# Kernel optimization log

Measured on AMD Instinct MI355X. Metric: run time of the kernel, lower is better.

The kernel has to match this reference:

```python
import jax, jax.numpy as jnp
import numpy as np

B, S, E, H, D = 2, 2048, 1024, 16, 64

def setup_inputs() -> dict:
    key = jax.random.key(0)
    ks = jax.random.split(key, 6)
    scale = 0.02
    x  = jax.random.normal(ks[0], (B, S, E), dtype=jnp.float32)
    Wq = jax.random.normal(ks[1], (E, E), dtype=jnp.float32) * scale
    Wk = jax.random.normal(ks[2], (E, E), dtype=jnp.float32) * scale
    Wv = jax.random.normal(ks[3], (E, E), dtype=jnp.float32) * scale
    Wo = jax.random.normal(ks[4], (E, E), dtype=jnp.float32) * scale
    bo = jax.random.normal(ks[5], (E,), dtype=jnp.float32) * scale
    return {"x": x, "Wq": Wq, "Wk": Wk, "Wv": Wv, "Wo": Wo, "bo": bo}

def reference(x, Wq, Wk, Wv, Wo, bo):
    # Per-head Q/K/V projections: equivalent to concatenating H heads of size D.
    q = jnp.einsum('bse,ehd->bhsd', x, Wq.reshape(E, H, D))
    k = jnp.einsum('bse,ehd->bhsd', x, Wk.reshape(E, H, D))
    v = jnp.einsum('bse,ehd->bhsd', x, Wv.reshape(E, H, D))
    # Scaled dot-product attention with causal mask (tril), per head.
    scores = jnp.einsum('bhqd,bhkd->bhqk', q, k) * (D ** -0.5)  # [B,H,S,S]
    causal = jnp.tril(jnp.ones((S, S), dtype=bool))
    scores = jnp.where(causal, scores, jnp.float32(-jnp.inf))
    attn = jax.nn.softmax(scores, axis=-1)
    out = jnp.einsum('bhqk,bhkd->bhqd', attn, v)            # [B,H,S,D]
    out = out.transpose(0, 2, 1, 3).reshape(B, S, E)        # concat heads
    # Output projection (dropout prob = 0.0 -> identity).
    return out @ Wo + bo
```

## Files before the change

kernel.cpp:

```cpp
#include <hip/hip_runtime.h>
#include <hip/hip_bf16.h>
#include <cstdint>
#include <cstddef>

typedef unsigned short u16;
typedef unsigned int u32;
typedef __bf16 bf16x8 __attribute__((ext_vector_type(8)));
typedef float f32x4 __attribute__((ext_vector_type(4)));
typedef u32 u32x4 __attribute__((ext_vector_type(4)));
typedef u32 u32x2 __attribute__((ext_vector_type(2)));

constexpr int Bb = 2, Ss = 2048, Ee = 1024, Hh = 16, Dd = 64;
constexpr int Mm = Bb * Ss;
constexpr int NT = Ss / 64;

__device__ __forceinline__ u16 f2bf(float f) {
    union { float f; u32 u; } x; x.f = f;
    u32 r = x.u + 0x7fffu + ((x.u >> 16) & 1u);
    return (u16)(r >> 16);
}

__global__ __launch_bounds__(256) void k_f2b(
    const float* __restrict__ src, u16* __restrict__ dst)
{
    const int i = blockIdx.x * 256 + threadIdx.x;
    float4 v = reinterpret_cast<const float4*>(src)[i];
    ushort4 o;
    o.x = f2bf(v.x); o.y = f2bf(v.y); o.z = f2bf(v.z); o.w = f2bf(v.w);
    reinterpret_cast<ushort4*>(dst)[i] = o;
}

__global__ __launch_bounds__(256) void k_transpose(
    const float* __restrict__ Wq, const float* __restrict__ Wk,
    const float* __restrict__ Wv, const float* __restrict__ Wo,
    u16* __restrict__ WqkvT, u16* __restrict__ WoT)
{
    __shared__ float sm[32][33];
    const int z = blockIdx.z;
    const float* src = (z == 0) ? Wq : (z == 1) ? Wk : (z == 2) ? Wv : Wo;
    u16* dst = (z < 3) ? (WqkvT + (size_t)z * Ee * Ee) : WoT;
    const int kt = blockIdx.x * 32, nt = blockIdx.y * 32;
    const int tx = threadIdx.x, ty = threadIdx.y;
#pragma unroll
    for (int i = 0; i < 4; ++i)
        sm[ty + 8 * i][tx] = src[(size_t)(kt + ty + 8 * i) * Ee + nt + tx];
    __syncthreads();
#pragma unroll
    for (int i = 0; i < 4; ++i)
        dst[(size_t)(nt + ty + 8 * i) * Ee + kt + tx] = f2bf(sm[tx][ty + 8 * i]);
}

template <int MODE>
__global__ __launch_bounds__(256) void k_gemm(
    const u16* __restrict__ A, const u16* __restrict__ Bt,
    void* __restrict__ Cout, u16* __restrict__ vT,
    int K, const float* __restrict__ bias)
{
    __shared__ u16 As[128][40];
    __shared__ u16 Bs[128][40];
    const int bm = blockIdx.x * 128, bn = blockIdx.y * 128;
    const int tid = threadIdx.x;
    const int wave = tid >> 6, lane = tid & 63, quad = lane >> 4, l16 = lane & 15;
    const int wr = wave >> 1, wc = wave & 1;

    f32x4 acc[4][4] = {};

    for (int k0 = 0; k0 < K; k0 += 32) {
#pragma unroll
        for (int it = 0; it < 2; ++it) {
            int v = tid + it * 256;
            int r = v >> 2, g = v & 3;
            *reinterpret_cast<int4*>(&As[r][g * 8]) =
                *reinterpret_cast<const int4*>(A + (size_t)(bm + r) * K + k0 + g * 8);
            *reinterpret_cast<int4*>(&Bs[r][g * 8]) =
                *reinterpret_cast<const int4*>(Bt + (size_t)(bn + r) * K + k0 + g * 8);
        }
        __syncthreads();

        bf16x8 af[4], bfr[4];
#pragma unroll
        for (int mt = 0; mt < 4; ++mt)
            af[mt] = *reinterpret_cast<bf16x8*>(&As[wr * 64 + mt * 16 + l16][quad * 8]);
#pragma unroll
        for (int nt = 0; nt < 4; ++nt)
            bfr[nt] = *reinterpret_cast<bf16x8*>(&Bs[wc * 64 + nt * 16 + l16][quad * 8]);
#pragma unroll
        for (int mt = 0; mt < 4; ++mt)
#pragma unroll
            for (int nt = 0; nt < 4; ++nt)
                acc[mt][nt] = __builtin_amdgcn_mfma_f32_16x16x32_bf16(
                    af[mt], bfr[nt], acc[mt][nt], 0, 0, 0);
        __syncthreads();
    }

    if constexpr (MODE == 1) {
        float* C = (float*)Cout;
#pragma unroll
        for (int mt = 0; mt < 4; ++mt)
#pragma unroll
            for (int nt = 0; nt < 4; ++nt) {
                const int col = bn + wc * 64 + nt * 16 + l16;
                const float bv = bias[col];
#pragma unroll
                for (int r = 0; r < 4; ++r) {
                    const int row = bm + wr * 64 + mt * 16 + quad * 4 + r;
                    C[(size_t)row * Ee + col] = acc[mt][nt][r] + bv;
                }
            }
    } else {
        if (bn < 2 * Ee) {
            u16* C = (u16*)Cout;
#pragma unroll
            for (int mt = 0; mt < 4; ++mt)
#pragma unroll
                for (int nt = 0; nt < 4; ++nt) {
                    const int col = bn + wc * 64 + nt * 16 + l16;
#pragma unroll
                    for (int r = 0; r < 4; ++r) {
                        const int row = bm + wr * 64 + mt * 16 + quad * 4 + r;
                        C[(size_t)row * (2 * Ee) + col] = f2bf(acc[mt][nt][r]);
                    }
                }
        } else {
#pragma unroll
            for (int mt = 0; mt < 4; ++mt)
#pragma unroll
                for (int nt = 0; nt < 4; ++nt) {
                    const int vd = bn - 2 * Ee + wc * 64 + nt * 16 + l16;
                    const int h = vd >> 6, d = vd & 63;
#pragma unroll
                    for (int r = 0; r < 4; ++r) {
                        const int row = bm + wr * 64 + mt * 16 + quad * 4 + r;
                        const int b = row >> 11, s = row & 2047;
                        vT[(((size_t)b * Hh + h) * Dd + d) * Ss + s] = f2bf(acc[mt][nt][r]);
                    }
                }
        }
    }
}

__global__ __launch_bounds__(256) void k_attn(
    const u16* __restrict__ qk, const u16* __restrict__ vT,
    u16* __restrict__ attn_out)
{
    __shared__ u16 Qs[64][72];
    __shared__ u16 Ks[2][64][72];
    __shared__ u16 Vs[2][64][72];

    const int pair = blockIdx.x;
    const int bh = blockIdx.y;
    const int b = bh >> 4, h = bh & 15;
    const int tid = threadIdx.x;
    const int wave = tid >> 6, lane = tid & 63, quad = lane >> 4, l16 = lane & 15;
    const int r8 = tid >> 3, g8 = tid & 7;
    const size_t qkbase = (size_t)b * Ss * (2 * Ee);
    const size_t vbase  = ((size_t)(b * Hh + h) * Dd) * Ss;

    const int tiles[2] = { pair, NT - 1 - pair };
    constexpr float LOG2E = 1.4426950408889634f;
    constexpr float C1 = 0.125f * LOG2E;
    constexpr float C2 = 4.0f * LOG2E;

    for (int ph = 0; ph < 2; ++ph) {
        const int qt = tiles[ph];

#pragma unroll
        for (int hf = 0; hf < 2; ++hf) {
            const int rr = r8 + hf * 32;
            *reinterpret_cast<int4*>(&Qs[rr][g8 * 8]) = *reinterpret_cast<const int4*>(
                qk + qkbase + (size_t)(qt * 64 + rr) * (2 * Ee) + h * 64 + g8 * 8);
            *reinterpret_cast<int4*>(&Ks[0][rr][g8 * 8]) = *reinterpret_cast<const int4*>(
                qk + qkbase + (size_t)rr * (2 * Ee) + Ee + h * 64 + g8 * 8);
            *reinterpret_cast<int4*>(&Vs[0][rr][g8 * 8]) = *reinterpret_cast<const int4*>(
                vT + vbase + (size_t)rr * Ss + g8 * 8);
        }
        __syncthreads();

        const bf16x8 aq0 = *reinterpret_cast<bf16x8*>(&Qs[wave * 16 + l16][quad * 8]);
        const bf16x8 aq1 = *reinterpret_cast<bf16x8*>(&Qs[wave * 16 + l16][32 + quad * 8]);

        float l_lane = 0.f;
        f32x4 acc[4];
#pragma unroll
        for (int dt = 0; dt < 4; ++dt) acc[dt] = (f32x4){0.f, 0.f, 0.f, 0.f};

        for (int kt = 0; kt <= qt; ++kt) {
            const int cur = kt & 1, nxt = cur ^ 1;
            int4 kreg0, kreg1, vreg0, vreg1;
            if (kt < qt) {
                kreg0 = *reinterpret_cast<const int4*>(
                    qk + qkbase + (size_t)((kt + 1) * 64 + r8) * (2 * Ee) + Ee + h * 64 + g8 * 8);
                kreg1 = *reinterpret_cast<const int4*>(
                    qk + qkbase + (size_t)((kt + 1) * 64 + r8 + 32) * (2 * Ee) + Ee + h * 64 + g8 * 8);
                vreg0 = *reinterpret_cast<const int4*>(
                    vT + vbase + (size_t)r8 * Ss + (kt + 1) * 64 + g8 * 8);
                vreg1 = *reinterpret_cast<const int4*>(
                    vT + vbase + (size_t)(r8 + 32) * Ss + (kt + 1) * 64 + g8 * 8);
            }

            f32x4 sc[4];
#pragma unroll
            for (int ct = 0; ct < 4; ++ct) {
                bf16x8 bk0 = *reinterpret_cast<bf16x8*>(&Ks[cur][ct * 16 + l16][quad * 8]);
                bf16x8 bk1 = *reinterpret_cast<bf16x8*>(&Ks[cur][ct * 16 + l16][32 + quad * 8]);
                f32x4 z = {0.f, 0.f, 0.f, 0.f};
                z = __builtin_amdgcn_mfma_f32_16x16x32_bf16(bk0, aq0, z, 0, 0, 0);
                z = __builtin_amdgcn_mfma_f32_16x16x32_bf16(bk1, aq1, z, 0, 0, 0);
                sc[ct] = z;
            }

            u32 pb[4][4];
            if (kt == qt) {
#pragma unroll
                for (int ct = 0; ct < 4; ++ct)
#pragma unroll
                    for (int r = 0; r < 4; ++r) {
                        float t = sc[ct][r] * C1 - C2;
                        if (ct * 16 + quad * 4 + r > wave * 16 + l16) t = -INFINITY;
                        union { float f; u32 u; } p; p.f = exp2f(t);
                        pb[ct][r] = p.u & 0xffff0000u;
                        p.u = pb[ct][r];
                        l_lane += p.f;
                    }
            } else {
#pragma unroll
                for (int ct = 0; ct < 4; ++ct)
#pragma unroll
                    for (int r = 0; r < 4; ++r) {
                        union { float f; u32 u; } p; p.f = exp2f(sc[ct][r] * C1 - C2);
                        pb[ct][r] = p.u & 0xffff0000u;
                        p.u = pb[ct][r];
                        l_lane += p.f;
                    }
            }

#pragma unroll
            for (int p2 = 0; p2 < 2; ++p2) {
                u32x4 bw;
                bw[0] = (pb[2 * p2][0] >> 16) | pb[2 * p2][1];
                bw[1] = (pb[2 * p2][2] >> 16) | pb[2 * p2][3];
                bw[2] = (pb[2 * p2 + 1][0] >> 16) | pb[2 * p2 + 1][1];
                bw[3] = (pb[2 * p2 + 1][2] >> 16) | pb[2 * p2 + 1][3];
                const bf16x8 pf = __builtin_bit_cast(bf16x8, bw);
#pragma unroll
                for (int dt = 0; dt < 4; ++dt) {
                    u32x2 lo = *reinterpret_cast<u32x2*>(&Vs[cur][dt * 16 + l16][p2 * 32 + quad * 4]);
                    u32x2 hi = *reinterpret_cast<u32x2*>(&Vs[cur][dt * 16 + l16][p2 * 32 + 16 + quad * 4]);
                    u32x4 aw = {lo[0], lo[1], hi[0], hi[1]};
                    const bf16x8 vf = __builtin_bit_cast(bf16x8, aw);
                    acc[dt] = __builtin_amdgcn_mfma_f32_16x16x32_bf16(vf, pf, acc[dt], 0, 0, 0);
                }
            }

            if (kt < qt) {
                *reinterpret_cast<int4*>(&Ks[nxt][r8][g8 * 8]) = kreg0;
                *reinterpret_cast<int4*>(&Ks[nxt][r8 + 32][g8 * 8]) = kreg1;
                *reinterpret_cast<int4*>(&Vs[nxt][r8][g8 * 8]) = vreg0;
                *reinterpret_cast<int4*>(&Vs[nxt][r8 + 32][g8 * 8]) = vreg1;
            }
            __syncthreads();
        }

        l_lane += __shfl_xor(l_lane, 16);
        l_lane += __shfl_xor(l_lane, 32);
        const float inv = 1.0f / l_lane;
        const int row = qt * 64 + wave * 16 + l16;
#pragma unroll
        for (int dt = 0; dt < 4; ++dt) {
            ushort4 o;
            o.x = f2bf(acc[dt][0] * inv);
            o.y = f2bf(acc[dt][1] * inv);
            o.z = f2bf(acc[dt][2] * inv);
            o.w = f2bf(acc[dt][3] * inv);
            *reinterpret_cast<ushort4*>(
                &attn_out[((size_t)b * Ss + row) * Ee + h * 64 + dt * 16 + quad * 4]) = o;
        }
    }
}

extern "C" void kernel_launch(void* const* d_in, const int* in_sizes, int n_in,
                              void* d_out, int out_size, void* d_ws, size_t ws_size,
                              hipStream_t stream)
{
    const float* x  = (const float*)d_in[0];
    const float* Wq = (const float*)d_in[1];
    const float* Wk = (const float*)d_in[2];
    const float* Wv = (const float*)d_in[3];
    const float* Wo = (const float*)d_in[4];
    const float* bo = (const float*)d_in[5];
    float* out = (float*)d_out;

    u16* xb    = (u16*)d_ws;
    u16* WqkvT = xb + (size_t)Mm * Ee;
    u16* WoT   = WqkvT + (size_t)3 * Ee * Ee;
    u16* qk    = WoT + (size_t)Ee * Ee;
    u16* vT    = qk + (size_t)Mm * 2 * Ee;
    u16* attn  = vT + (size_t)Bb * Hh * Dd * Ss;
    const size_t need = ((size_t)Mm * Ee + (size_t)3 * Ee * Ee + (size_t)Ee * Ee +
                         (size_t)Mm * 2 * Ee + (size_t)Bb * Hh * Dd * Ss +
                         (size_t)Mm * Ee) * sizeof(u16);
    if (ws_size < need) return;

    k_f2b<<<dim3(Mm * Ee / 4 / 256), 256, 0, stream>>>(x, xb);
    k_transpose<<<dim3(32, 32, 4), dim3(32, 8), 0, stream>>>(Wq, Wk, Wv, Wo, WqkvT, WoT);
    k_gemm<2><<<dim3(Mm / 128, 3 * Ee / 128), 256, 0, stream>>>(xb, WqkvT, qk, vT, Ee, nullptr);
    k_attn<<<dim3(NT / 2, Bb * Hh), 256, 0, stream>>>(qk, vT, attn);
    k_gemm<1><<<dim3(Mm / 128, Ee / 128), 256, 0, stream>>>(attn, WoT, out, nullptr, Ee, bo);
}
```

Measured before the change: 194.8 us.

## Fuse preprocessing kernels, use direct global-to-LDS loads, and coalesce V-transpose stores

Merges the x bf16 conversion and the weight transposes into one launch, with an extra z-slice handling the conversion. The GEMM tile loads now use global_load_lds to write straight into unpadded LDS tiles instead of passing through registers. The V-transposed epilogue goes through a per-wave LDS buffer so stores become 16-byte coalesced rows rather than scattered 2-byte writes. Side effects: the GEMM LDS tiles lose their padding, which may cause bank conflicts on fragment reads, and the loop still uses single buffering with barriers.

New measurement: 190.0 us. 2.5% less time.

```diff
diff --git a/kernel.cpp b/kernel.cpp
--- a/kernel.cpp
+++ b/kernel.cpp
@@ -20,27 +20,37 @@
     return (u16)(r >> 16);
 }
 
-__global__ __launch_bounds__(256) void k_f2b(
-    const float* __restrict__ src, u16* __restrict__ dst)
-{
-    const int i = blockIdx.x * 256 + threadIdx.x;
-    float4 v = reinterpret_cast<const float4*>(src)[i];
-    ushort4 o;
-    o.x = f2bf(v.x); o.y = f2bf(v.y); o.z = f2bf(v.z); o.w = f2bf(v.w);
-    reinterpret_cast<ushort4*>(dst)[i] = o;
-}
-
-__global__ __launch_bounds__(256) void k_transpose(
+typedef __attribute__((address_space(3))) void lds_void_t;
+typedef const __attribute__((address_space(1))) void gbl_void_t;
+__device__ __forceinline__ void gload_lds16(const u16* g, u16* l) {
+    __builtin_amdgcn_global_load_lds((gbl_void_t*)g, (lds_void_t*)l, 16, 0, 0);
+}
+
+__global__ __launch_bounds__(256) void k_pre(
+    const float* __restrict__ x,
     const float* __restrict__ Wq, const float* __restrict__ Wk,
     const float* __restrict__ Wv, const float* __restrict__ Wo,
-    u16* __restrict__ WqkvT, u16* __restrict__ WoT)
+    u16* __restrict__ xb, u16* __restrict__ WqkvT, u16* __restrict__ WoT)
 {
+    const int z = blockIdx.z;
+    const int tx = threadIdx.x, ty = threadIdx.y;
+    if (z == 4) {
+        const int tid = ty * 32 + tx;
+        const size_t base = ((size_t)blockIdx.y * 32 + blockIdx.x) * 4096;
+#pragma unroll
+        for (int it = 0; it < 4; ++it) {
+            const size_t i = base / 4 + it * 256 + tid;
+            float4 v = reinterpret_cast<const float4*>(x)[i];
+            ushort4 o;
+            o.x = f2bf(v.x); o.y = f2bf(v.y); o.z = f2bf(v.z); o.w = f2bf(v.w);
+            reinterpret_cast<ushort4*>(xb)[i] = o;
+        }
+        return;
+    }
     __shared__ float sm[32][33];
-    const int z = blockIdx.z;
     const float* src = (z == 0) ? Wq : (z == 1) ? Wk : (z == 2) ? Wv : Wo;
     u16* dst = (z < 3) ? (WqkvT + (size_t)z * Ee * Ee) : WoT;
     const int kt = blockIdx.x * 32, nt = blockIdx.y * 32;
-    const int tx = threadIdx.x, ty = threadIdx.y;
 #pragma unroll
     for (int i = 0; i < 4; ++i)
         sm[ty + 8 * i][tx] = src[(size_t)(kt + ty + 8 * i) * Ee + nt + tx];
@@ -56,25 +66,27 @@
     void* __restrict__ Cout, u16* __restrict__ vT,
     int K, const float* __restrict__ bias)
 {
-    __shared__ u16 As[128][40];
-    __shared__ u16 Bs[128][40];
+    __shared__ u16 As[128][32];
+    __shared__ u16 Bs[128][32];
+    __shared__ u16 Tw[4][16][68];
     const int bm = blockIdx.x * 128, bn = blockIdx.y * 128;
     const int tid = threadIdx.x;
     const int wave = tid >> 6, lane = tid & 63, quad = lane >> 4, l16 = lane & 15;
     const int wr = wave >> 1, wc = wave & 1;
 
+    const int ldrow = lane >> 2, ldcol = (lane & 3) * 8;
+    const u16* gA = A + (size_t)(bm + wave * 32 + ldrow) * K + ldcol;
+    const u16* gB = Bt + (size_t)(bn + wave * 32 + ldrow) * K + ldcol;
+    u16* lA = &As[wave * 32][0];
+    u16* lB = &Bs[wave * 32][0];
+
     f32x4 acc[4][4] = {};
 
     for (int k0 = 0; k0 < K; k0 += 32) {
-#pragma unroll
-        for (int it = 0; it < 2; ++it) {
-            int v = tid + it * 256;
-            int r = v >> 2, g = v & 3;
-            *reinterpret_cast<int4*>(&As[r][g * 8]) =
-                *reinterpret_cast<const int4*>(A + (size_t)(bm + r) * K + k0 + g * 8);
-            *reinterpret_cast<int4*>(&Bs[r][g * 8]) =
-                *reinterpret_cast<const int4*>(Bt + (size_t)(bn + r) * K + k0 + g * 8);
-        }
+        gload_lds16(gA + k0, lA);
+        gload_lds16(gA + k0 + 16 * K, lA + 16 * 32);
+        gload_lds16(gB + k0, lB);
+        gload_lds16(gB + k0 + 16 * K, lB + 16 * 32);
         __syncthreads();
 
         bf16x8 af[4], bfr[4];
@@ -122,19 +134,25 @@
                     }
                 }
         } else {
-#pragma unroll
-            for (int mt = 0; mt < 4; ++mt)
-#pragma unroll
-                for (int nt = 0; nt < 4; ++nt) {
-                    const int vd = bn - 2 * Ee + wc * 64 + nt * 16 + l16;
-                    const int h = vd >> 6, d = vd & 63;
-#pragma unroll
-                    for (int r = 0; r < 4; ++r) {
-                        const int row = bm + wr * 64 + mt * 16 + quad * 4 + r;
-                        const int b = row >> 11, s = row & 2047;
-                        vT[(((size_t)b * Hh + h) * Dd + d) * Ss + s] = f2bf(acc[mt][nt][r]);
-                    }
-                }
+            const int m_base = bm + wr * 64;
+            const int b = m_base >> 11, s0 = m_base & 2047;
+            const int rw = lane >> 2, cg = (lane & 3) * 16;
+#pragma unroll
+            for (int nt = 0; nt < 4; ++nt) {
+#pragma unroll
+                for (int mt = 0; mt < 4; ++mt)
+#pragma unroll
+                    for (int r = 0; r < 4; ++r)
+                        Tw[wave][l16][mt * 16 + quad * 4 + r] = f2bf(acc[mt][nt][r]);
+                __asm__ volatile("s_waitcnt lgkmcnt(0)" ::: "memory");
+                const int vd = bn - 2 * Ee + wc * 64 + nt * 16 + rw;
+                u16* dst = vT + ((size_t)(b * Hh + (vd >> 6)) * Dd + (vd & 63)) * Ss + s0 + cg;
+                int4 a0 = *reinterpret_cast<int4*>(&Tw[wave][rw][cg]);
+                int4 a1 = *reinterpret_cast<int4*>(&Tw[wave][rw][cg + 8]);
+                *reinterpret_cast<int4*>(dst) = a0;
+                *reinterpret_cast<int4*>(dst + 8) = a1;
+                __asm__ volatile("s_waitcnt lgkmcnt(0)" ::: "memory");
+            }
         }
     }
 }
@@ -301,8 +319,7 @@
                          (size_t)Mm * Ee) * sizeof(u16);
     if (ws_size < need) return;
 
-    k_f2b<<<dim3(Mm * Ee / 4 / 256), 256, 0, stream>>>(x, xb);
-    k_transpose<<<dim3(32, 32, 4), dim3(32, 8), 0, stream>>>(Wq, Wk, Wv, Wo, WqkvT, WoT);
+    k_pre<<<dim3(32, 32, 5), dim3(32, 8), 0, stream>>>(x, Wq, Wk, Wv, Wo, xb, WqkvT, WoT);
     k_gemm<2><<<dim3(Mm / 128, 3 * Ee / 128), 256, 0, stream>>>(xb, WqkvT, qk, vT, Ee, nullptr);
     k_attn<<<dim3(NT / 2, Bb * Hh), 256, 0, stream>>>(qk, vT, attn);
     k_gemm<1><<<dim3(Mm / 128, Ee / 128), 256, 0, stream>>>(attn, WoT, out, nullptr, Ee, bo);
```
